# Optimization experiments

Measured on AMD Instinct MI355X. Metric: run time of the kernel, lower is better.

The kernel has to match this reference:

```python
import jax, jax.numpy as jnp
import numpy as np

NH = 1024
VS = 50257
CUT0 = 1675          # round(VS/30)
CUT1 = 3 * CUT0      # 5025
N_CLUSTERS = 2
HEAD_SIZE = CUT0 + N_CLUSTERS          # 1677
D0, D1 = NH // 4, NH // 16             # 256, 64
SZ0, SZ1 = CUT1 - CUT0, VS - CUT1      # 3350, 45232


def setup_inputs() -> dict:
    key = jax.random.key(0)
    ks = jax.random.split(key, 8)
    s = 0.02
    return {
        "x": jax.random.normal(ks[0], (8, 512, NH), dtype=jnp.float32),
        "y": jax.random.randint(ks[1], (8, 512), 0, VS, dtype=jnp.int64),
        "head_w": jax.random.normal(ks[2], (HEAD_SIZE, NH), dtype=jnp.float32) * s,
        "head_b": jnp.zeros((HEAD_SIZE,), dtype=jnp.float32),
        "proj0": jax.random.normal(ks[3], (D0, NH), dtype=jnp.float32) * s,
        "w0": jax.random.normal(ks[4], (SZ0, D0), dtype=jnp.float32) * s,
        "proj1": jax.random.normal(ks[5], (D1, NH), dtype=jnp.float32) * s,
        "w1": jax.random.normal(ks[6], (SZ1, D1), dtype=jnp.float32) * s,
    }


def reference(x, y, head_w, head_b, proj0, w0, proj1, w1):
    # Flatten as in the torch forward: x -> [N, nh], y -> [N]
    xf = x.reshape(-1, x.shape[-1])            # [N, NH]
    yf = y.reshape(-1)                         # [N]

    # Head: shortlist tokens + 2 cluster logits
    head_logits = jnp.einsum('nh,vh->nv', xf, head_w) + head_b   # [N, 1677]
    head_lp = jax.nn.log_softmax(head_logits, axis=-1)

    # Default: target in head shortlist
    in_head = yf < CUT0
    idx_head = jnp.where(in_head, yf, 0)
    out = jnp.take_along_axis(head_lp, idx_head[:, None], axis=1)[:, 0]

    # Tail clusters: dense per-cluster small GEMMs + log-softmax, masked select
    for i, (low, high, proj, w) in enumerate(
            [(CUT0, CUT1, proj0, w0), (CUT1, VS, proj1, w1)]):
        size = high - low
        h = jnp.einsum('nh,dh->nd', xf, proj)          # [N, d_i]
        lp = jax.nn.log_softmax(jnp.einsum('nd,vd->nv', h, w), axis=-1)  # [N, size]
        rel = jnp.clip(yf - low, 0, size - 1)
        cl = head_lp[:, CUT0 + i] + jnp.take_along_axis(lp, rel[:, None], axis=1)[:, 0]
        mask = (yf >= low) & (yf < high)
        out = jnp.where(mask, cl, out)

    loss = -jnp.mean(out)
    return out, loss
```

## Files before the change

### kernel.cpp

```cpp
#include <hip/hip_runtime.h>
#include <stdint.h>

#define NROWS 4096
#define NHID 1024
#define CC0 1675
#define CC1 5025
#define HEADSZ 1677
#define PD0 256
#define PD1 64
#define TSZ0 3350
#define TSZ1 45232
#define HPN (HEADSZ + PD0 + PD1)
#define TPC1 6
#define L2E 1.4426950408889634f
#define LN2 0.6931471805599453f

#define NB_HD 448
#define NB_PJ 96
#define NB_CW 512
#define NB_MID (NB_HD + NB_PJ + NB_CW)

#define NB_C1 1888
#define NB_C0 864
#define NB_TG 1024
#define NB_TAIL (NB_C1 + NB_C0 + NB_TG)

typedef __attribute__((ext_vector_type(8))) __bf16 bf16x8;
typedef __attribute__((ext_vector_type(4))) float f32x4;

__device__ __forceinline__ unsigned short f2bf(float f) {
  union { float f; uint32_t u; } v; v.f = f;
  return (unsigned short)((v.u + 0x7FFFu + ((v.u >> 16) & 1u)) >> 16);
}
__device__ __forceinline__ float bfl(uint32_t u) {
  union { uint32_t u; float f; } v; v.u = u << 16; return v.f;
}
__device__ __forceinline__ float bfh(uint32_t u) {
  union { uint32_t u; float f; } v; v.u = u & 0xFFFF0000u; return v.f;
}
__device__ __forceinline__ float bf1(unsigned short u) {
  union { uint32_t u; float f; } v; v.u = ((uint32_t)u) << 16; return v.f;
}
#define EXP2(x) __builtin_amdgcn_exp2f(x)

#define CV1 1048576
#define CV2 1477888
#define CV3 1543424
#define CV4 1559808
#define CV5 1774208
#define CV6 2497920
#define CVW0 (CV5 - CV4)
#define CVW  (CV6 - CV4)

__global__ void conv_part(const float* __restrict__ x, const float* __restrict__ hw,
                          const float* __restrict__ p0, const float* __restrict__ p1,
                          unsigned short* __restrict__ dst,
                          const int* __restrict__ y,
                          int* __restrict__ idx0, int* __restrict__ pos0,
                          int* __restrict__ idx1, int* __restrict__ pos1,
                          int* __restrict__ n01) {
  if (blockIdx.x == 1024) {
    __shared__ int sc0[256], sc1[256], nsh[2];
    int t = threadIdx.x;
    int yl[16];
    int c0 = 0, c1 = 0;
#pragma unroll
    for (int k = 0; k < 16; ++k) {
      int yv = y[t * 16 + k];
      yl[k] = yv;
      c0 += (yv >= CC0 && yv < CC1);
      c1 += (yv >= CC1);
    }
    sc0[t] = c0; sc1[t] = c1;
    __syncthreads();
    if (t == 0) {
      int a0 = 0, a1 = 0;
      for (int i = 0; i < 256; ++i) {
        int v0 = sc0[i]; sc0[i] = a0; a0 += v0;
        int v1 = sc1[i]; sc1[i] = a1; a1 += v1;
      }
      n01[0] = a0; n01[1] = a1; nsh[0] = a0; nsh[1] = a1;
    }
    __syncthreads();
    int p0c = sc0[t], p1c = sc1[t];
#pragma unroll
    for (int k = 0; k < 16; ++k) {
      int n = t * 16 + k, yv = yl[k];
      if (yv >= CC0 && yv < CC1) { idx0[p0c] = n; pos0[n] = p0c; ++p0c; }
      else if (yv >= CC1)        { idx1[p1c] = n; pos1[n] = p1c; ++p1c; }
    }
    for (int j = nsh[0] + t; j < NROWS; j += 256) idx0[j] = 0;
    for (int j = nsh[1] + t; j < NROWS; j += 256) idx1[j] = 0;
    return;
  }
  const int stride = 1024 * 256;
  for (int i = blockIdx.x * 256 + threadIdx.x; i < CV4; i += stride) {
    const float* src; int off; float sc;
    if (i < CV1)      { src = x;  off = i;       sc = 1.f; }
    else if (i < CV2) { src = hw; off = i - CV1; sc = L2E; }
    else if (i < CV3) { src = p0; off = i - CV2; sc = 1.f; }
    else              { src = p1; off = i - CV3; sc = 1.f; }
    float4 v = reinterpret_cast<const float4*>(src)[off];
    ushort4 o;
    o.x = f2bf(v.x * sc); o.y = f2bf(v.y * sc);
    o.z = f2bf(v.z * sc); o.w = f2bf(v.w * sc);
    reinterpret_cast<ushort4*>(dst)[i] = o;
  }
}

#define GLOAD(g, l) __builtin_amdgcn_global_load_lds( \
    (const __attribute__((address_space(1))) uint32_t*)(const void*)(g), \
    (__attribute__((address_space(3))) uint32_t*)(void*)(l), 16, 0, 0)

#define SWZB(L) ((L) ^ ((((L) >> 7) & 7) << 4))

__device__ __forceinline__
void gemm_core(const unsigned short* __restrict__ A, int lda,
               const unsigned short* __restrict__ B, int ldb,
               int N, int K, int tile0, int tile1, int brow,
               const float* __restrict__ bias,
               float* __restrict__ sum_out,
               unsigned short* __restrict__ Cout, int ldc, int coutStart,
               unsigned short* AsB, unsigned short* BsB,
               const int* __restrict__ gidx) {
  const int tid = threadIdx.x;
  const int lane = tid & 63;
  const int wid = tid >> 6;
  const int wrow = (wid >> 1) * 64;
  const int wcol = (wid & 1) * 64;
  const int lr = lane & 15, lg = lane >> 4;
  const int nsteps = (tile1 - tile0) * (K >> 5);
  const int rowBase = brow + wrow;

  int arowc[2];
#pragma unroll
  for (int c = 0; c < 2; ++c) {
    int g = wid * 128 + c * 64 + lane;
    int S = SWZB(g * 16);
    int row = S >> 6;
    arowc[c] = gidx ? gidx[brow + row] : brow + row;
  }

  float sacc[4][4];
#pragma unroll
  for (int m = 0; m < 4; ++m)
#pragma unroll
    for (int r = 0; r < 4; ++r) sacc[m][r] = 0.f;

  auto stage = [&](int b, int tt, int kk) {
#pragma unroll
    for (int c = 0; c < 2; ++c) {
      int g = wid * 128 + c * 64 + lane;
      int L = g * 16;
      int S = SWZB(L);
      int row = S >> 6, ko = (S >> 4) & 3;
      GLOAD(A + (size_t)arowc[c] * lda + kk + ko * 8, (char*)AsB + b * 8192 + L);
      int bsrc = tt * 128 + row; bsrc = bsrc < N ? bsrc : N - 1;
      GLOAD(B + (size_t)bsrc * ldb + kk + ko * 8, (char*)BsB + b * 8192 + L);
    }
  };

  f32x4 acc[4][4];
#pragma unroll
  for (int m = 0; m < 4; ++m)
#pragma unroll
    for (int n = 0; n < 4; ++n) acc[m][n] = (f32x4){0.f, 0.f, 0.f, 0.f};

  int tp = tile0, kp = 0;
  auto adv = [&](int& t, int& k) { k += 32; if (k == K) { k = 0; ++t; } };
  stage(0, tp, kp); adv(tp, kp);
  if (nsteps > 1) { stage(1, tp, kp); adv(tp, kp); }

  int tile = tile0, k0 = 0;
  for (int s = 0; s < nsteps; ++s) {
    if (s + 1 < nsteps) asm volatile("s_waitcnt vmcnt(4)" ::: "memory");
    else                asm volatile("s_waitcnt vmcnt(0)" ::: "memory");
    __builtin_amdgcn_s_barrier();
    if (s + 2 < nsteps) { stage((s + 2) % 3, tp, kp); adv(tp, kp); }

    const int cur = s % 3;
    int k0n = k0 + 32, tn = tile;
    if (k0n == K) { k0n = 0; tn = tile + 1; }

    bf16x8 af[4], bfv[4];
#pragma unroll
    for (int m = 0; m < 4; ++m)
      af[m] = *(const bf16x8*)((const char*)AsB + cur * 8192 +
                               SWZB((wrow + m * 16 + lr) * 64 + lg * 16));
#pragma unroll
    for (int n = 0; n < 4; ++n)
      bfv[n] = *(const bf16x8*)((const char*)BsB + cur * 8192 +
                                SWZB((wcol + n * 16 + lr) * 64 + lg * 16));
#pragma unroll
    for (int m = 0; m < 4; ++m)
#pragma unroll
      for (int n = 0; n < 4; ++n)
        acc[m][n] = __builtin_amdgcn_mfma_f32_16x16x32_bf16(af[m], bfv[n], acc[m][n], 0, 0, 0);

    if (tn != tile) {
      const int cb = tile * 128 + wcol;
#pragma unroll
      for (int m = 0; m < 4; ++m)
#pragma unroll
        for (int n = 0; n < 4; ++n) {
#pragma unroll
          for (int r = 0; r < 4; ++r) {
            int col = cb + n * 16 + lr;
            if (col < N) {
              float v = acc[m][n][r];
              if (Cout && col >= coutStart) {
                int row = rowBase + m * 16 + lg * 4 + r;
                Cout[(size_t)row * ldc + (col - coutStart)] = f2bf(v);
              } else {
                if (bias) v = fmaf(bias[col], L2E, v);
                sacc[m][r] += EXP2(v);
              }
            }
          }
          acc[m][n] = (f32x4){0.f, 0.f, 0.f, 0.f};
        }
    }
    tile = tn; k0 = k0n;
  }

#pragma unroll
  for (int m = 0; m < 4; ++m)
#pragma unroll
    for (int r = 0; r < 4; ++r) {
      float s = sacc[m][r];
      s += __shfl_xor(s, 1); s += __shfl_xor(s, 2);
      s += __shfl_xor(s, 4); s += __shfl_xor(s, 8);
      if (lr == 0) atomicAdd(&sum_out[rowBase + m * 16 + lg * 4 + r], s);
    }
}

__global__ __launch_bounds__(256, 3)
void fused_mid(const unsigned short* __restrict__ xb,
               const unsigned short* __restrict__ hpb,
               const float* __restrict__ head_b,
               float* __restrict__ hs,
               unsigned short* __restrict__ hb,
               float* __restrict__ dm,
               const float* __restrict__ w0f, const float* __restrict__ w1f,
               unsigned short* __restrict__ dstAll) {
  __shared__ __align__(16) unsigned short lds[6 * 4096];
  const int bid = blockIdx.x;

  if (bid < NB_HD) {
    const int xcd = bid & 7;
    const int local = bid >> 3;
    const int rowBlk = xcd * 4 + local / 14;
    const int colChunk = local % 14;
    gemm_core(xb, NHID, hpb, NHID, HEADSZ, NHID, colChunk, colChunk + 1,
              rowBlk * 128, head_b, hs, nullptr, 0, 0,
              lds, lds + 3 * 4096, nullptr);
    return;
  }

  if (bid < NB_HD + NB_PJ) {
    const int b1 = bid - NB_HD;
    const int cpx = NB_PJ >> 3;
    const int sid = (b1 & 7) * cpx + (b1 >> 3);
    const int rowBlk = sid & 31;
    const int colChunk = sid >> 5;
    gemm_core(xb, NHID, hpb + (size_t)HEADSZ * NHID, NHID, PD0 + PD1, NHID,
              colChunk, colChunk + 1, rowBlk * 128,
              nullptr, dm, hb, PD0 + PD1, 0, lds, lds + 3 * 4096, nullptr);
    return;
  }

  {
    const int b2 = bid - NB_HD - NB_PJ;
    const int stride = NB_CW * 256;
    for (int i = b2 * 256 + (int)threadIdx.x; i < CVW; i += stride) {
      const float* src; int off;
      if (i < CVW0) { src = w0f; off = i; }
      else          { src = w1f; off = i - CVW0; }
      float4 v = reinterpret_cast<const float4*>(src)[off];
      ushort4 o;
      o.x = f2bf(v.x * L2E); o.y = f2bf(v.y * L2E);
      o.z = f2bf(v.z * L2E); o.w = f2bf(v.w * L2E);
      reinterpret_cast<ushort4*>(dstAll)[CV4 + i] = o;
    }
  }
}

__global__ __launch_bounds__(256, 3)
void fused_tail(const unsigned short* __restrict__ hb,
                const unsigned short* __restrict__ w0b,
                const unsigned short* __restrict__ w1b,
                const unsigned short* __restrict__ xb,
                const unsigned short* __restrict__ hwb,
                const float* __restrict__ head_b,
                const int* __restrict__ y,
                const int* __restrict__ idx0, const int* __restrict__ idx1,
                const int* __restrict__ n01,
                float* __restrict__ s0, float* __restrict__ s1,
                float* __restrict__ ht, float* __restrict__ tc) {
  __shared__ __align__(16) unsigned short lds[6 * 4096];
  const int bid = blockIdx.x;

  if (bid < NB_C1) {
    const int tid = threadIdx.x;
    const int lane = tid & 63;
    const int wid = tid >> 6;
    const int lr = lane & 15, lg = lane >> 4;
    const int cpx = NB_C1 >> 3;
    const int sid = (bid & 7) * cpx + (bid >> 3);
    const int rowBlk = sid & 31;
    const int colChunk = sid >> 5;
    if (rowBlk * 128 >= n01[1]) return;
    const int rowBase = rowBlk * 128 + (wid >> 1) * 64;
    const int wcol = (wid & 1) * 64;
    const int tile0 = colChunk * TPC1;

    int colOff[4], srcOff[4];
#pragma unroll
    for (int c = 0; c < 4; ++c) {
      int L = (c * 256 + tid) * 16;
      int S = L ^ (((L >> 7) & 7) << 4);
      colOff[c] = S >> 7;
      srcOff[c] = (S & 127) >> 1;
    }
    auto stage = [&](int b, int t) {
#pragma unroll
      for (int c = 0; c < 4; ++c) {
        int gc = t * 128 + colOff[c];
        gc = gc < TSZ1 ? gc : TSZ1 - 1;
        GLOAD(w1b + (size_t)gc * PD1 + srcOff[c],
              (char*)lds + b * 16384 + (c * 256 + tid) * 16);
      }
    };

    bf16x8 af[4][2];
#pragma unroll
    for (int m = 0; m < 4; ++m) {
      int ridx = idx1[rowBase + m * 16 + lr];
      const unsigned short* p = hb + PD0 +
          (size_t)ridx * (PD0 + PD1) + lg * 8;
      af[m][0] = *(const bf16x8*)p;
      af[m][1] = *(const bf16x8*)(p + 32);
    }

    float sacc[4][4];
#pragma unroll
    for (int m = 0; m < 4; ++m)
#pragma unroll
      for (int r = 0; r < 4; ++r) sacc[m][r] = 0.f;

    stage(0, tile0);
    stage(1, tile0 + 1);

#pragma unroll 1
    for (int s = 0; s < TPC1; ++s) {
      if (s + 1 < TPC1) asm volatile("s_waitcnt vmcnt(4)" ::: "memory");
      else              asm volatile("s_waitcnt vmcnt(0)" ::: "memory");
      __builtin_amdgcn_s_barrier();
      if (s + 2 < TPC1) stage((s + 2) % 3, tile0 + s + 2);

      const int cur = s % 3;
      const int cb = (tile0 + s) * 128 + wcol;
      const int full = (cb + 63 < TSZ1);

#pragma unroll
      for (int nh = 0; nh < 2; ++nh) {
        bf16x8 bf[2][2];
#pragma unroll
        for (int nn = 0; nn < 2; ++nn) {
          int ccol = wcol + (nh * 2 + nn) * 16 + lr;
#pragma unroll
          for (int kh = 0; kh < 2; ++kh) {
            int L = ccol * 128 + kh * 64 + lg * 16;
            bf[nn][kh] = *(const bf16x8*)((const char*)lds + cur * 16384 +
                                          (L ^ ((ccol & 7) << 4)));
          }
        }
        f32x4 acc[4][2];
#pragma unroll
        for (int m = 0; m < 4; ++m)
#pragma unroll
          for (int nn = 0; nn < 2; ++nn) {
            f32x4 a = (f32x4){0.f, 0.f, 0.f, 0.f};
            a = __builtin_amdgcn_mfma_f32_16x16x32_bf16(af[m][0], bf[nn][0], a, 0, 0, 0);
            a = __builtin_amdgcn_mfma_f32_16x16x32_bf16(af[m][1], bf[nn][1], a, 0, 0, 0);
            acc[m][nn] = a;
          }
        if (full) {
#pragma unroll
          for (int m = 0; m < 4; ++m)
#pragma unroll
            for (int r = 0; r < 4; ++r)
              sacc[m][r] += EXP2(acc[m][0][r]) + EXP2(acc[m][1][r]);
        } else {
#pragma unroll
          for (int m = 0; m < 4; ++m)
#pragma unroll
            for (int r = 0; r < 4; ++r) {
              float t = 0.f;
#pragma unroll
              for (int nn = 0; nn < 2; ++nn)
                if (cb + (nh * 2 + nn) * 16 + lr < TSZ1) t += EXP2(acc[m][nn][r]);
              sacc[m][r] += t;
            }
        }
      }
    }

#pragma unroll
    for (int m = 0; m < 4; ++m)
#pragma unroll
      for (int r = 0; r < 4; ++r) {
        float s = sacc[m][r];
        s += __shfl_xor(s, 1); s += __shfl_xor(s, 2);
        s += __shfl_xor(s, 4); s += __shfl_xor(s, 8);
        if (lr == 0) atomicAdd(&s1[rowBase + m * 16 + lg * 4 + r], s);
      }
    return;
  }

  if (bid < NB_C1 + NB_C0) {
    const int b0 = bid - NB_C1;
    const int cpx = NB_C0 >> 3;
    const int sid = (b0 & 7) * cpx + (b0 >> 3);
    const int rowBlk = sid & 31;
    const int colChunk = sid >> 5;
    if (rowBlk * 128 >= n01[0]) return;
    gemm_core(hb, PD0 + PD1, w0b, PD0, TSZ0, PD0, colChunk, colChunk + 1,
              rowBlk * 128, nullptr, s0, nullptr, 0, 0,
              lds, lds + 3 * 4096, idx0);
    return;
  }

  {
    const int b2 = bid - NB_C1 - NB_C0;
    int row = b2 * 4 + (threadIdx.x >> 6);
    int lane = threadIdx.x & 63;
    int yv = y[row];
    int th = yv < CC0 ? yv : (yv < CC1 ? CC0 : CC0 + 1);

    const unsigned short* xr = xb + (size_t)row * NHID + lane * 16;
    const unsigned short* wr = hwb + (size_t)th * NHID + lane * 16;
    uint4 xa = *(const uint4*)xr,       wa = *(const uint4*)wr;
    uint4 xc = *(const uint4*)(xr + 8), wc = *(const uint4*)(wr + 8);
    float s = 0.f;
    uint32_t xs[8] = {xa.x, xa.y, xa.z, xa.w, xc.x, xc.y, xc.z, xc.w};
    uint32_t ws[8] = {wa.x, wa.y, wa.z, wa.w, wc.x, wc.y, wc.z, wc.w};
#pragma unroll
    for (int j = 0; j < 8; ++j)
      s += bfl(xs[j]) * bfl(ws[j]) + bfh(xs[j]) * bfh(ws[j]);
#pragma unroll
    for (int d = 1; d < 64; d <<= 1) s += __shfl_xor(s, d);

    float cl = 0.f;
    if (yv >= CC0) {
      if (yv < CC1) {
        int rel = yv - CC0;
        const unsigned short* hr = hb + (size_t)row * (PD0 + PD1) + lane * 4;
        const unsigned short* w0r = w0b + (size_t)rel * PD0 + lane * 4;
        uint2 ha = *(const uint2*)hr, wa0 = *(const uint2*)w0r;
        cl = bfl(ha.x) * bfl(wa0.x) + bfh(ha.x) * bfh(wa0.x)
           + bfl(ha.y) * bfl(wa0.y) + bfh(ha.y) * bfh(wa0.y);
      } else {
        int rel = yv - CC1;
        cl = bf1(hb[(size_t)row * (PD0 + PD1) + PD0 + lane])
           * bf1(w1b[(size_t)rel * PD1 + lane]);
      }
#pragma unroll
      for (int d = 1; d < 64; d <<= 1) cl += __shfl_xor(cl, d);
    }
    if (lane == 0) { ht[row] = s * LN2 + head_b[th]; tc[row] = (yv < CC0) ? 0.f : cl; }
  }
}

__global__ void rowloss(const float* __restrict__ hs, const float* __restrict__ ht,
                        const float* __restrict__ s0, const float* __restrict__ s1,
                        const float* __restrict__ tc,
                        const int* __restrict__ pos0, const int* __restrict__ pos1,
                        const int* __restrict__ y, float* __restrict__ out) {
  int n = blockIdx.x * 256 + threadIdx.x;
  int yv = y[n];
  float o = ht[n] - __builtin_amdgcn_logf(hs[n]) * LN2;
  if (yv >= CC0) {
    float sv = (yv < CC1) ? s0[pos0[n]] : s1[pos1[n]];
    o += tc[n] * LN2 - __builtin_amdgcn_logf(sv) * LN2;
  }
  out[n] = o;
  float l = o;
#pragma unroll
  for (int d = 1; d < 64; d <<= 1) l += __shfl_xor(l, d);
  __shared__ float red[4];
  if ((threadIdx.x & 63) == 0) red[threadIdx.x >> 6] = l;
  __syncthreads();
  if (threadIdx.x == 0)
    atomicAdd(&out[NROWS], -(red[0] + red[1] + red[2] + red[3]) / (float)NROWS);
}

extern "C" void kernel_launch(void* const* d_in, const int* in_sizes, int n_in,
                              void* d_out, int out_size, void* d_ws, size_t ws_size,
                              hipStream_t stream) {
  const float* x      = (const float*)d_in[0];
  const int*   y      = (const int*)d_in[1];
  const float* head_w = (const float*)d_in[2];
  const float* head_b = (const float*)d_in[3];
  const float* proj0  = (const float*)d_in[4];
  const float* w0     = (const float*)d_in[5];
  const float* proj1  = (const float*)d_in[6];
  const float* w1     = (const float*)d_in[7];
  float* out = (float*)d_out;

  char* wp = (char*)d_ws;
  unsigned short* xb  = (unsigned short*)wp; wp += (size_t)NROWS * NHID * 2;
  unsigned short* hpb = (unsigned short*)wp; wp += (size_t)HPN * NHID * 2;
  unsigned short* w0b = (unsigned short*)wp; wp += (size_t)TSZ0 * PD0 * 2;
  unsigned short* w1b = (unsigned short*)wp; wp += (size_t)TSZ1 * PD1 * 2;
  unsigned short* hb  = (unsigned short*)wp; wp += (size_t)NROWS * (PD0 + PD1) * 2;
  float* hs = (float*)wp; wp += NROWS * 4;
  float* s0 = (float*)wp; wp += NROWS * 4;
  float* s1 = (float*)wp; wp += NROWS * 4;
  float* ht = (float*)wp; wp += NROWS * 4;
  float* tc = (float*)wp; wp += NROWS * 4;
  float* dm = (float*)wp; wp += NROWS * 4;
  int* idx0 = (int*)wp; wp += NROWS * 4;
  int* pos0 = (int*)wp; wp += NROWS * 4;
  int* idx1 = (int*)wp; wp += NROWS * 4;
  int* pos1 = (int*)wp; wp += NROWS * 4;
  int* n01  = (int*)wp; wp += 8 * 4;

  hipMemsetAsync(hs, 0, 3 * NROWS * 4, stream);
  hipMemsetAsync(out + NROWS, 0, 4, stream);

  conv_part<<<dim3(1025), 256, 0, stream>>>(
      x, head_w, proj0, proj1, xb, y, idx0, pos0, idx1, pos1, n01);

  fused_mid<<<dim3(NB_MID), 256, 0, stream>>>(
      xb, hpb, head_b, hs, hb, dm, w0, w1, xb);

  fused_tail<<<dim3(NB_TAIL), 256, 0, stream>>>(
      hb, w0b, w1b, xb, hpb, head_b, y, idx0, idx1, n01, s0, s1, ht, tc);

  rowloss<<<dim3(NROWS / 256), 256, 0, stream>>>(
      hs, ht, s0, s1, tc, pos0, pos1, y, out);
}
```

Baseline: 105.0 us.

## Move head GEMM into tail kernel and coarsen cluster-1 and target blocks

Moves the head logits GEMM blocks out of the mid kernel into the tail kernel, so it runs alongside the tail cluster GEMMs rather than before them. This shortens the critical mid stage and balances work across the two launches. Cluster-1 blocks now each process 15 tiles instead of 6 (768 blocks instead of 1888), with a bound for the last partial chunk. Target-gather blocks each loop over 8 rows per wave. The cost is fewer, longer blocks, which risks tail imbalance and less latency hiding.

```diff
diff --git a/kernel.cpp b/kernel.cpp
--- a/kernel.cpp
+++ b/kernel.cpp
@@ -11,19 +11,20 @@
 #define TSZ0 3350
 #define TSZ1 45232
 #define HPN (HEADSZ + PD0 + PD1)
-#define TPC1 6
+#define NT1 354
+#define TPC1 15
 #define L2E 1.4426950408889634f
 #define LN2 0.6931471805599453f
 
-#define NB_HD 448
 #define NB_PJ 96
 #define NB_CW 512
-#define NB_MID (NB_HD + NB_PJ + NB_CW)
-
-#define NB_C1 1888
+#define NB_MID (NB_PJ + NB_CW)
+
+#define NB_HD 448
+#define NB_C1 768
 #define NB_C0 864
-#define NB_TG 1024
-#define NB_TAIL (NB_C1 + NB_C0 + NB_TG)
+#define NB_TG 128
+#define NB_TAIL (NB_HD + NB_C1 + NB_C0 + NB_TG)
 
 typedef __attribute__((ext_vector_type(8))) __bf16 bf16x8;
 typedef __attribute__((ext_vector_type(4))) float f32x4;
@@ -237,8 +238,6 @@
 __global__ __launch_bounds__(256, 3)
 void fused_mid(const unsigned short* __restrict__ xb,
                const unsigned short* __restrict__ hpb,
-               const float* __restrict__ head_b,
-               float* __restrict__ hs,
                unsigned short* __restrict__ hb,
                float* __restrict__ dm,
                const float* __restrict__ w0f, const float* __restrict__ w1f,
@@ -246,21 +245,9 @@
   __shared__ __align__(16) unsigned short lds[6 * 4096];
   const int bid = blockIdx.x;
 
-  if (bid < NB_HD) {
-    const int xcd = bid & 7;
-    const int local = bid >> 3;
-    const int rowBlk = xcd * 4 + local / 14;
-    const int colChunk = local % 14;
-    gemm_core(xb, NHID, hpb, NHID, HEADSZ, NHID, colChunk, colChunk + 1,
-              rowBlk * 128, head_b, hs, nullptr, 0, 0,
-              lds, lds + 3 * 4096, nullptr);
-    return;
-  }
-
-  if (bid < NB_HD + NB_PJ) {
-    const int b1 = bid - NB_HD;
+  if (bid < NB_PJ) {
     const int cpx = NB_PJ >> 3;
-    const int sid = (b1 & 7) * cpx + (b1 >> 3);
+    const int sid = (bid & 7) * cpx + (bid >> 3);
     const int rowBlk = sid & 31;
     const int colChunk = sid >> 5;
     gemm_core(xb, NHID, hpb + (size_t)HEADSZ * NHID, NHID, PD0 + PD1, NHID,
@@ -270,7 +257,7 @@
   }
 
   {
-    const int b2 = bid - NB_HD - NB_PJ;
+    const int b2 = bid - NB_PJ;
     const int stride = NB_CW * 256;
     for (int i = b2 * 256 + (int)threadIdx.x; i < CVW; i += stride) {
       const float* src; int off;
@@ -295,24 +282,39 @@
                 const int* __restrict__ y,
                 const int* __restrict__ idx0, const int* __restrict__ idx1,
                 const int* __restrict__ n01,
+                float* __restrict__ hs,
                 float* __restrict__ s0, float* __restrict__ s1,
                 float* __restrict__ ht, float* __restrict__ tc) {
   __shared__ __align__(16) unsigned short lds[6 * 4096];
   const int bid = blockIdx.x;
 
-  if (bid < NB_C1) {
+  if (bid < NB_HD) {
+    const int xcd = bid & 7;
+    const int local = bid >> 3;
+    const int rowBlk = xcd * 4 + local / 14;
+    const int colChunk = local % 14;
+    gemm_core(xb, NHID, hwb, NHID, HEADSZ, NHID, colChunk, colChunk + 1,
+              rowBlk * 128, head_b, hs, nullptr, 0, 0,
+              lds, lds + 3 * 4096, nullptr);
+    return;
+  }
+
+  if (bid < NB_HD + NB_C1) {
+    const int b1 = bid - NB_HD;
     const int tid = threadIdx.x;
     const int lane = tid & 63;
     const int wid = tid >> 6;
     const int lr = lane & 15, lg = lane >> 4;
     const int cpx = NB_C1 >> 3;
-    const int sid = (bid & 7) * cpx + (bid >> 3);
+    const int sid = (b1 & 7) * cpx + (b1 >> 3);
     const int rowBlk = sid & 31;
     const int colChunk = sid >> 5;
     if (rowBlk * 128 >= n01[1]) return;
     const int rowBase = rowBlk * 128 + (wid >> 1) * 64;
     const int wcol = (wid & 1) * 64;
     const int tile0 = colChunk * TPC1;
+    const int tile1 = min(tile0 + TPC1, NT1);
+    const int nt = tile1 - tile0;
 
     int colOff[4], srcOff[4];
 #pragma unroll
@@ -349,14 +351,14 @@
       for (int r = 0; r < 4; ++r) sacc[m][r] = 0.f;
 
     stage(0, tile0);
-    stage(1, tile0 + 1);
+    if (nt > 1) stage(1, tile0 + 1);
 
 #pragma unroll 1
-    for (int s = 0; s < TPC1; ++s) {
-      if (s + 1 < TPC1) asm volatile("s_waitcnt vmcnt(4)" ::: "memory");
-      else              asm volatile("s_waitcnt vmcnt(0)" ::: "memory");
+    for (int s = 0; s < nt; ++s) {
+      if (s + 1 < nt) asm volatile("s_waitcnt vmcnt(4)" ::: "memory");
+      else            asm volatile("s_waitcnt vmcnt(0)" ::: "memory");
       __builtin_amdgcn_s_barrier();
-      if (s + 2 < TPC1) stage((s + 2) % 3, tile0 + s + 2);
+      if (s + 2 < nt) stage((s + 2) % 3, tile0 + s + 2);
 
       const int cur = s % 3;
       const int cb = (tile0 + s) * 128 + wcol;
@@ -418,8 +420,8 @@
     return;
   }
 
-  if (bid < NB_C1 + NB_C0) {
-    const int b0 = bid - NB_C1;
+  if (bid < NB_HD + NB_C1 + NB_C0) {
+    const int b0 = bid - NB_HD - NB_C1;
     const int cpx = NB_C0 >> 3;
     const int sid = (b0 & 7) * cpx + (b0 >> 3);
     const int rowBlk = sid & 31;
@@ -432,43 +434,46 @@
   }
 
   {
-    const int b2 = bid - NB_C1 - NB_C0;
-    int row = b2 * 4 + (threadIdx.x >> 6);
+    const int b2 = bid - NB_HD - NB_C1 - NB_C0;
     int lane = threadIdx.x & 63;
-    int yv = y[row];
-    int th = yv < CC0 ? yv : (yv < CC1 ? CC0 : CC0 + 1);
-
-    const unsigned short* xr = xb + (size_t)row * NHID + lane * 16;
-    const unsigned short* wr = hwb + (size_t)th * NHID + lane * 16;
-    uint4 xa = *(const uint4*)xr,       wa = *(const uint4*)wr;
-    uint4 xc = *(const uint4*)(xr + 8), wc = *(const uint4*)(wr + 8);
-    float s = 0.f;
-    uint32_t xs[8] = {xa.x, xa.y, xa.z, xa.w, xc.x, xc.y, xc.z, xc.w};
-    uint32_t ws[8] = {wa.x, wa.y, wa.z, wa.w, wc.x, wc.y, wc.z, wc.w};
-#pragma unroll
-    for (int j = 0; j < 8; ++j)
-      s += bfl(xs[j]) * bfl(ws[j]) + bfh(xs[j]) * bfh(ws[j]);
-#pragma unroll
-    for (int d = 1; d < 64; d <<= 1) s += __shfl_xor(s, d);
-
-    float cl = 0.f;
-    if (yv >= CC0) {
-      if (yv < CC1) {
-        int rel = yv - CC0;
-        const unsigned short* hr = hb + (size_t)row * (PD0 + PD1) + lane * 4;
-        const unsigned short* w0r = w0b + (size_t)rel * PD0 + lane * 4;
-        uint2 ha = *(const uint2*)hr, wa0 = *(const uint2*)w0r;
-        cl = bfl(ha.x) * bfl(wa0.x) + bfh(ha.x) * bfh(wa0.x)
-           + bfl(ha.y) * bfl(wa0.y) + bfh(ha.y) * bfh(wa0.y);
-      } else {
-        int rel = yv - CC1;
-        cl = bf1(hb[(size_t)row * (PD0 + PD1) + PD0 + lane])
-           * bf1(w1b[(size_t)rel * PD1 + lane]);
+#pragma unroll 1
+    for (int it = 0; it < 8; ++it) {
+      int row = b2 * 32 + (int)(threadIdx.x >> 6) * 8 + it;
+      int yv = y[row];
+      int th = yv < CC0 ? yv : (yv < CC1 ? CC0 : CC0 + 1);
+
+      const unsigned short* xr = xb + (size_t)row * NHID + lane * 16;
+      const unsigned short* wr = hwb + (size_t)th * NHID + lane * 16;
+      uint4 xa = *(const uint4*)xr,       wa = *(const uint4*)wr;
+      uint4 xc = *(const uint4*)(xr + 8), wc = *(const uint4*)(wr + 8);
+      float s = 0.f;
+      uint32_t xs[8] = {xa.x, xa.y, xa.z, xa.w, xc.x, xc.y, xc.z, xc.w};
+      uint32_t ws[8] = {wa.x, wa.y, wa.z, wa.w, wc.x, wc.y, wc.z, wc.w};
+#pragma unroll
+      for (int j = 0; j < 8; ++j)
+        s += bfl(xs[j]) * bfl(ws[j]) + bfh(xs[j]) * bfh(ws[j]);
+#pragma unroll
+      for (int d = 1; d < 64; d <<= 1) s += __shfl_xor(s, d);
+
+      float cl = 0.f;
+      if (yv >= CC0) {
+        if (yv < CC1) {
+          int rel = yv - CC0;
+          const unsigned short* hr = hb + (size_t)row * (PD0 + PD1) + lane * 4;
+          const unsigned short* w0r = w0b + (size_t)rel * PD0 + lane * 4;
+          uint2 ha = *(const uint2*)hr, wa0 = *(const uint2*)w0r;
+          cl = bfl(ha.x) * bfl(wa0.x) + bfh(ha.x) * bfh(wa0.x)
+             + bfl(ha.y) * bfl(wa0.y) + bfh(ha.y) * bfh(wa0.y);
+        } else {
+          int rel = yv - CC1;
+          cl = bf1(hb[(size_t)row * (PD0 + PD1) + PD0 + lane])
+             * bf1(w1b[(size_t)rel * PD1 + lane]);
+        }
+#pragma unroll
+        for (int d = 1; d < 64; d <<= 1) cl += __shfl_xor(cl, d);
       }
-#pragma unroll
-      for (int d = 1; d < 64; d <<= 1) cl += __shfl_xor(cl, d);
-    }
-    if (lane == 0) { ht[row] = s * LN2 + head_b[th]; tc[row] = (yv < CC0) ? 0.f : cl; }
+      if (lane == 0) { ht[row] = s * LN2 + head_b[th]; tc[row] = (yv < CC0) ? 0.f : cl; }
+    }
   }
 }
 
@@ -533,10 +538,10 @@
       x, head_w, proj0, proj1, xb, y, idx0, pos0, idx1, pos1, n01);
 
   fused_mid<<<dim3(NB_MID), 256, 0, stream>>>(
-      xb, hpb, head_b, hs, hb, dm, w0, w1, xb);
+      xb, hpb, hb, dm, w0, w1, xb);
 
   fused_tail<<<dim3(NB_TAIL), 256, 0, stream>>>(
-      hb, w0b, w1b, xb, hpb, head_b, y, idx0, idx1, n01, s0, s1, ht, tc);
+      hb, w0b, w1b, xb, hpb, head_b, y, idx0, idx1, n01, hs, s0, s1, ht, tc);
 
   rowloss<<<dim3(NROWS / 256), 256, 0, stream>>>(
       hs, ht, s0, s1, tc, pos0, pos1, y, out);
```

New measurement: 108.5 us. 3.3% more time.

## Use double-buffered K64 GEMM core with larger LDS tiles in mid kernel

Applied to the files above, without the earlier changes.

Adds a second GEMM core for the head and projection GEMMs in the mid kernel. Each step now loads a K=64 slice into two 16 KB ping-pong LDS buffers per operand, replacing the previous tile scheme. The aim is to halve the number of K iterations and barriers while overlapping global loads with MFMA work. In exchange, LDS per block grows to 64 KB and launch bounds drop from 3 to 2 blocks per CU, which lowers occupancy. The unused dummy sum buffer for the projection path is also removed.

```diff
diff --git a/kernel.cpp b/kernel.cpp
--- a/kernel.cpp
+++ b/kernel.cpp
@@ -234,16 +234,120 @@
     }
 }
 
-__global__ __launch_bounds__(256, 3)
+__device__ __forceinline__
+void gemm_core2(const unsigned short* __restrict__ A, int lda,
+                const unsigned short* __restrict__ B, int ldb,
+                int N, int K, int tile0, int brow,
+                const float* __restrict__ bias,
+                float* __restrict__ sum_out,
+                unsigned short* __restrict__ Cout, int ldc, int coutStart,
+                char* AsB, char* BsB) {
+  const int tid = threadIdx.x;
+  const int lane = tid & 63;
+  const int wid = tid >> 6;
+  const int wrow = (wid >> 1) * 64;
+  const int wcol = (wid & 1) * 64;
+  const int lr = lane & 15, lg = lane >> 4;
+  const int nsteps = K >> 6;
+  const int rowBase = brow + wrow;
+
+  auto stage = [&](int b, int kk) {
+#pragma unroll
+    for (int c = 0; c < 4; ++c) {
+      int L = (c * 256 + tid) * 16;
+      int kh = L >> 13;
+      int L8 = L & 8191;
+      int S = SWZB(L8);
+      int row = S >> 6, ko = (S >> 4) & 3;
+      int koff = kk + kh * 32 + ko * 8;
+      GLOAD(A + (size_t)(brow + row) * lda + koff, AsB + b * 16384 + L);
+      int bsrc = tile0 * 128 + row; bsrc = bsrc < N ? bsrc : N - 1;
+      GLOAD(B + (size_t)bsrc * ldb + koff, BsB + b * 16384 + L);
+    }
+  };
+
+  f32x4 acc[4][4];
+#pragma unroll
+  for (int m = 0; m < 4; ++m)
+#pragma unroll
+    for (int n = 0; n < 4; ++n) acc[m][n] = (f32x4){0.f, 0.f, 0.f, 0.f};
+
+  stage(0, 0);
+  asm volatile("s_waitcnt vmcnt(0)" ::: "memory");
+  __builtin_amdgcn_s_barrier();
+
+  for (int s = 0; s < nsteps; ++s) {
+    if (s + 1 < nsteps) stage((s + 1) & 1, (s + 1) * 64);
+    const int cur = s & 1;
+#pragma unroll
+    for (int kh = 0; kh < 2; ++kh) {
+      bf16x8 af[4], bfv[4];
+#pragma unroll
+      for (int m = 0; m < 4; ++m)
+        af[m] = *(const bf16x8*)(AsB + cur * 16384 + kh * 8192 +
+                                 SWZB((wrow + m * 16 + lr) * 64 + lg * 16));
+#pragma unroll
+      for (int n = 0; n < 4; ++n)
+        bfv[n] = *(const bf16x8*)(BsB + cur * 16384 + kh * 8192 +
+                                  SWZB((wcol + n * 16 + lr) * 64 + lg * 16));
+#pragma unroll
+      for (int m = 0; m < 4; ++m)
+#pragma unroll
+        for (int n = 0; n < 4; ++n)
+          acc[m][n] = __builtin_amdgcn_mfma_f32_16x16x32_bf16(af[m], bfv[n], acc[m][n], 0, 0, 0);
+    }
+    if (s + 1 < nsteps) {
+      asm volatile("s_waitcnt vmcnt(0)" ::: "memory");
+      __builtin_amdgcn_s_barrier();
+    }
+  }
+
+  const int cb = tile0 * 128 + wcol;
+  float sacc[4][4];
+#pragma unroll
+  for (int m = 0; m < 4; ++m)
+#pragma unroll
+    for (int r = 0; r < 4; ++r) sacc[m][r] = 0.f;
+#pragma unroll
+  for (int m = 0; m < 4; ++m)
+#pragma unroll
+    for (int n = 0; n < 4; ++n)
+#pragma unroll
+      for (int r = 0; r < 4; ++r) {
+        int col = cb + n * 16 + lr;
+        if (col < N) {
+          float v = acc[m][n][r];
+          if (Cout && col >= coutStart) {
+            int row = rowBase + m * 16 + lg * 4 + r;
+            Cout[(size_t)row * ldc + (col - coutStart)] = f2bf(v);
+          } else {
+            if (bias) v = fmaf(bias[col], L2E, v);
+            sacc[m][r] += EXP2(v);
+          }
+        }
+      }
+  if (sum_out) {
+#pragma unroll
+    for (int m = 0; m < 4; ++m)
+#pragma unroll
+      for (int r = 0; r < 4; ++r) {
+        float s = sacc[m][r];
+        s += __shfl_xor(s, 1); s += __shfl_xor(s, 2);
+        s += __shfl_xor(s, 4); s += __shfl_xor(s, 8);
+        if (lr == 0) atomicAdd(&sum_out[rowBase + m * 16 + lg * 4 + r], s);
+      }
+  }
+}
+
+__global__ __launch_bounds__(256, 2)
 void fused_mid(const unsigned short* __restrict__ xb,
                const unsigned short* __restrict__ hpb,
                const float* __restrict__ head_b,
                float* __restrict__ hs,
                unsigned short* __restrict__ hb,
-               float* __restrict__ dm,
                const float* __restrict__ w0f, const float* __restrict__ w1f,
                unsigned short* __restrict__ dstAll) {
-  __shared__ __align__(16) unsigned short lds[6 * 4096];
+  __shared__ __align__(16) char lds[65536];
   const int bid = blockIdx.x;
 
   if (bid < NB_HD) {
@@ -251,9 +355,8 @@
     const int local = bid >> 3;
     const int rowBlk = xcd * 4 + local / 14;
     const int colChunk = local % 14;
-    gemm_core(xb, NHID, hpb, NHID, HEADSZ, NHID, colChunk, colChunk + 1,
-              rowBlk * 128, head_b, hs, nullptr, 0, 0,
-              lds, lds + 3 * 4096, nullptr);
+    gemm_core2(xb, NHID, hpb, NHID, HEADSZ, NHID, colChunk, rowBlk * 128,
+               head_b, hs, nullptr, 0, 0, lds, lds + 32768);
     return;
   }
 
@@ -263,9 +366,9 @@
     const int sid = (b1 & 7) * cpx + (b1 >> 3);
     const int rowBlk = sid & 31;
     const int colChunk = sid >> 5;
-    gemm_core(xb, NHID, hpb + (size_t)HEADSZ * NHID, NHID, PD0 + PD1, NHID,
-              colChunk, colChunk + 1, rowBlk * 128,
-              nullptr, dm, hb, PD0 + PD1, 0, lds, lds + 3 * 4096, nullptr);
+    gemm_core2(xb, NHID, hpb + (size_t)HEADSZ * NHID, NHID, PD0 + PD1, NHID,
+               colChunk, rowBlk * 128,
+               nullptr, nullptr, hb, PD0 + PD1, 0, lds, lds + 32768);
     return;
   }
 
@@ -427,7 +530,7 @@
     if (rowBlk * 128 >= n01[0]) return;
     gemm_core(hb, PD0 + PD1, w0b, PD0, TSZ0, PD0, colChunk, colChunk + 1,
               rowBlk * 128, nullptr, s0, nullptr, 0, 0,
-              lds, lds + 3 * 4096, idx0);
+              (unsigned short*)lds, (unsigned short*)lds + 3 * 4096, idx0);
     return;
   }
 
@@ -519,7 +622,6 @@
   float* s1 = (float*)wp; wp += NROWS * 4;
   float* ht = (float*)wp; wp += NROWS * 4;
   float* tc = (float*)wp; wp += NROWS * 4;
-  float* dm = (float*)wp; wp += NROWS * 4;
   int* idx0 = (int*)wp; wp += NROWS * 4;
   int* pos0 = (int*)wp; wp += NROWS * 4;
   int* idx1 = (int*)wp; wp += NROWS * 4;
@@ -533,7 +635,7 @@
       x, head_w, proj0, proj1, xb, y, idx0, pos0, idx1, pos1, n01);
 
   fused_mid<<<dim3(NB_MID), 256, 0, stream>>>(
-      xb, hpb, head_b, hs, hb, dm, w0, w1, xb);
+      xb, hpb, head_b, hs, hb, w0, w1, xb);
 
   fused_tail<<<dim3(NB_TAIL), 256, 0, stream>>>(
       hb, w0b, w1b, xb, hpb, head_b, y, idx0, idx1, n01, s0, s1, ht, tc);
```

Result: faster. 102.9 us (-2.0%).
